# Kernel optimization log

Measured on AMD Instinct MI355X. Metric: run time of the kernel, lower is better.

The kernel has to match this reference:

```python
import jax, jax.numpy as jnp
import numpy as np

B, C_IN, C_OUT, F, K = 4, 64, 64, 50000, 16
BN_EPS = 1e-5


def setup_inputs() -> dict:
    key = jax.random.key(0)
    k1, k2, k3, k4 = jax.random.split(key, 4)
    fea = jax.random.normal(k1, (B, C_IN, F), dtype=jnp.float32)
    ring_n = jax.random.randint(k2, (B, F, K), 0, F, dtype=jnp.int64)
    # Conv1d(kernel_size=1) weight [out, in] and bias [out]
    W = jax.random.normal(k3, (C_OUT, C_IN), dtype=jnp.float32) / np.sqrt(C_IN)
    b = jax.random.normal(k4, (C_OUT,), dtype=jnp.float32) * 0.01
    gamma = jnp.ones((C_OUT,), dtype=jnp.float32)
    beta = jnp.zeros((C_OUT,), dtype=jnp.float32)
    return {"fea": fea, "ring_n": ring_n, "W": W, "b": b, "gamma": gamma, "beta": beta}


def reference(fea, ring_n, W, b, gamma, beta):
    # Note: original torch code overwrites the cat result, so only the
    # NEIGHBOR features are summed (center face excluded).
    def gather_sum(f, r):  # f: [C, F], r: [F, K]
        return f[:, r].sum(axis=-1)  # [C, F, K] -> [C, F]

    summed = jax.vmap(gather_sum)(fea, ring_n)  # [B, C_in, F]
    # 1x1 conv == channel matmul
    y = jnp.einsum("oc,bcf->bof", W, summed) + b[None, :, None]  # [B, C_out, F]
    # BatchNorm1d (training mode): stats over (batch, faces) per channel
    mean = y.mean(axis=(0, 2), keepdims=True)
    var = y.var(axis=(0, 2), keepdims=True)  # biased, as torch BN uses for normalization
    y = (y - mean) * jax.lax.rsqrt(var + BN_EPS)
    y = y * gamma[None, :, None] + beta[None, :, None]
    return jax.nn.relu(y)
```

## Files before the change

kernel.cpp:

```cpp
#include <hip/hip_runtime.h>
#include <hip/hip_bf16.h>
#include <stdint.h>

#define Bn 4
#define Cn 64
#define Fn 50000
#define Kn 16
#define NTOT (Bn*Fn)
#define EPS 1e-5f

typedef unsigned short u16;
typedef unsigned int u32;
typedef __attribute__((ext_vector_type(8))) short short8;
typedef __attribute__((ext_vector_type(4))) float f32x4;

__device__ __forceinline__ u16 f2bf(float x) {
  __hip_bfloat16 h = __float2bfloat16(x);
  return *reinterpret_cast<u16*>(&h);
}
__device__ __forceinline__ u32 pack2(float a, float b) {
  return (u32)f2bf(a) | ((u32)f2bf(b) << 16);
}
__device__ __forceinline__ void gload_lds16(const float* g, float* l) {
  __builtin_amdgcn_global_load_lds(
      (const __attribute__((address_space(1))) u32*)(g),
      (__attribute__((address_space(3))) u32*)(l), 16, 0, 0);
}

__global__ __launch_bounds__(256) void k1_mfma(
    const float* __restrict__ fea, const float* __restrict__ W,
    u32* __restrict__ Gt, float* __restrict__ gsum) {
  const int b = blockIdx.y;
  const int f0 = blockIdx.x * 128;
  const int t = threadIdx.x;
  const int l = t & 63;
  const int quad = l >> 4;
  const int lane15 = l & 15;
  const int wv = t >> 6;
  __shared__ float a_s[64 * 128];

  if (blockIdx.x == 0 && b == 0 && t < 128) gsum[t] = 0.f;

  {
    const float* fb = fea + (size_t)b * Cn * Fn;
    #pragma unroll
    for (int i = 0; i < 8; i++) {
      const int ch = wv * 16 + 2 * i + (l >> 5);
      const int fblk = (l & 31) ^ ((((ch >> 3) & 3)) << 1);
      int fg = f0 + fblk * 4;
      if (fg >= Fn) fg = f0;
      gload_lds16(fb + (size_t)ch * Fn + fg, &a_s[(wv * 16 + 2 * i) * 128]);
    }
  }

  short8 afr[4][2];
  #pragma unroll
  for (int ot = 0; ot < 4; ot++) {
    #pragma unroll
    for (int kk = 0; kk < 2; kk++) {
      const float* wr = W + (ot * 16 + lane15) * 64 + kk * 32 + quad * 8;
      float4 wa = *(const float4*)wr;
      float4 wb = *(const float4*)(wr + 4);
      union { short8 v; u32 u[4]; } fr;
      fr.u[0] = pack2(wa.x, wa.y); fr.u[1] = pack2(wa.z, wa.w);
      fr.u[2] = pack2(wb.x, wb.y); fr.u[3] = pack2(wb.z, wb.w);
      afr[ot][kk] = fr.v;
    }
  }
  __syncthreads();

  f32x4 acc[4][2];
  #pragma unroll
  for (int ot = 0; ot < 4; ot++)
    #pragma unroll
    for (int ft = 0; ft < 2; ft++) acc[ot][ft] = (f32x4){0.f, 0.f, 0.f, 0.f};

  #pragma unroll
  for (int ft = 0; ft < 2; ft++) {
    const int fl = wv * 32 + ft * 16 + lane15;
    const int fsw = fl ^ (quad << 3);
    float x[16];
    #pragma unroll
    for (int j = 0; j < 8; j++) x[j] = a_s[(quad * 8 + j) * 128 + fsw];
    #pragma unroll
    for (int j = 0; j < 8; j++) x[8 + j] = a_s[(32 + quad * 8 + j) * 128 + fsw];
    union { short8 s; u32 u[4]; } b0, b1;
    #pragma unroll
    for (int p = 0; p < 4; p++) {
      b0.u[p] = pack2(x[2 * p], x[2 * p + 1]);
      b1.u[p] = pack2(x[8 + 2 * p], x[8 + 2 * p + 1]);
    }
    #pragma unroll
    for (int ot = 0; ot < 4; ot++) {
      acc[ot][ft] = __builtin_amdgcn_mfma_f32_16x16x32_bf16(afr[ot][0], b0.s, acc[ot][ft], 0, 0, 0);
      acc[ot][ft] = __builtin_amdgcn_mfma_f32_16x16x32_bf16(afr[ot][1], b1.s, acc[ot][ft], 0, 0, 0);
    }
  }

  #pragma unroll
  for (int ot = 0; ot < 4; ot++) {
    #pragma unroll
    for (int ft = 0; ft < 2; ft++) {
      int fg = f0 + wv * 32 + ft * 16 + lane15;
      if (fg < Fn) {
        uint2 pv;
        pv.x = pack2(acc[ot][ft][0], acc[ot][ft][1]);
        pv.y = pack2(acc[ot][ft][2], acc[ot][ft][3]);
        *(uint2*)(Gt + ((size_t)(b * 4 + ot) * Fn + fg) * 8 + quad * 2) = pv;
      }
    }
  }
}

template<int WRITE_BF16>
__global__ __launch_bounds__(256) void k2_gather(
    const u32* __restrict__ Gt, const int* __restrict__ ring,
    const float* __restrict__ bias, u32* __restrict__ Y, float* __restrict__ outF,
    float* __restrict__ gsum, float* __restrict__ gsum2) {
  const int bid = blockIdx.x;
  const int combo = bid & 15;
  const int ft = bid >> 4;
  const int b = combo >> 2;
  const int seg = combo & 3;
  const int t = threadIdx.x;
  const int face_l = t >> 1;
  const int half = t & 1;
  const int fa = ft * 128 + face_l;
  const bool valid = fa < Fn;

  __shared__ float y_s[128][17];
  __shared__ float rs[16][17];
  __shared__ float rs2[16][17];

  float acc[8];
  #pragma unroll
  for (int i = 0; i < 8; i++) acc[i] = 0.f;

  const int c0 = seg * 16 + half * 8;
  float bv[8];
  #pragma unroll
  for (int i = 0; i < 8; i++) bv[i] = bias[c0 + i];

  if (valid) {
    const int4* rp = (const int4*)(ring + ((size_t)b * Fn + fa) * Kn);
    int4 i0 = rp[0], i1 = rp[1], i2 = rp[2], i3 = rp[3];
    int idx[16] = {i0.x,i0.y,i0.z,i0.w, i1.x,i1.y,i1.z,i1.w,
                   i2.x,i2.y,i2.z,i2.w, i3.x,i3.y,i3.z,i3.w};
    const uint4* Gs = (const uint4*)(Gt + (size_t)combo * Fn * 8);
    uint4 v[8], w[8];
    #pragma unroll
    for (int k = 0; k < 8; k++) v[k] = Gs[(size_t)idx[k] * 2 + half];
    #pragma unroll
    for (int k = 0; k < 8; k++) w[k] = Gs[(size_t)idx[8 + k] * 2 + half];
    #pragma unroll
    for (int k = 0; k < 8; k++) {
      u32 uu[4] = {v[k].x, v[k].y, v[k].z, v[k].w};
      #pragma unroll
      for (int p = 0; p < 4; p++) {
        acc[2*p]   += __uint_as_float(uu[p] << 16);
        acc[2*p+1] += __uint_as_float(uu[p] & 0xffff0000u);
      }
    }
    #pragma unroll
    for (int k = 0; k < 8; k++) {
      u32 uu[4] = {w[k].x, w[k].y, w[k].z, w[k].w};
      #pragma unroll
      for (int p = 0; p < 4; p++) {
        acc[2*p]   += __uint_as_float(uu[p] << 16);
        acc[2*p+1] += __uint_as_float(uu[p] & 0xffff0000u);
      }
    }
  }
  #pragma unroll
  for (int i = 0; i < 8; i++) acc[i] = valid ? acc[i] + bv[i] : 0.f;
  #pragma unroll
  for (int i = 0; i < 8; i++) y_s[face_l][half * 8 + i] = acc[i];
  __syncthreads();

  if (WRITE_BF16) {
    const int fp = t & 63, chb = t >> 6;
    const int fa2 = ft * 64 + fp;
    if (fa2 * 2 < Fn) {
      #pragma unroll
      for (int j = 0; j < 4; j++) {
        int ch = chb * 4 + j;
        Y[((size_t)b * 64 + seg * 16 + ch) * (Fn / 2) + fa2] =
            pack2(y_s[fp * 2][ch], y_s[fp * 2 + 1][ch]);
      }
    }
  } else {
    const int fl2 = t & 127, chb = t >> 7;
    if (ft * 128 + fl2 < Fn) {
      float* ob = outF + ((size_t)b * 64 + seg * 16 + chb * 8) * Fn + ft * 128 + fl2;
      #pragma unroll
      for (int j = 0; j < 8; j++) ob[(size_t)j * Fn] = y_s[fl2][chb * 8 + j];
    }
  }

  {
    const int ch = t & 15, part = t >> 4;
    float s = 0.f, s2 = 0.f;
    #pragma unroll
    for (int i = 0; i < 8; i++) {
      float v = y_s[part * 8 + i][ch];
      s += v; s2 += v * v;
    }
    rs[part][ch] = s; rs2[part][ch] = s2;
  }
  __syncthreads();
  if (t < 16) {
    float s = 0.f;
    #pragma unroll
    for (int p = 0; p < 16; p++) s += rs[p][t];
    atomicAdd(&gsum[seg * 16 + t], s);
  } else if (t < 32) {
    const int ch = t - 16;
    float s2 = 0.f;
    #pragma unroll
    for (int p = 0; p < 16; p++) s2 += rs2[p][ch];
    atomicAdd(&gsum2[seg * 16 + ch], s2);
  }
}

__global__ void k3_stats(const float* __restrict__ gsum, const float* __restrict__ gsum2,
                         const float* __restrict__ gamma, const float* __restrict__ beta,
                         float* __restrict__ ab) {
  int o = threadIdx.x;
  if (o < 64) {
    float inv = 1.0f / (float)NTOT;
    float mean = gsum[o] * inv;
    float var = gsum2[o] * inv - mean * mean;
    float r = rsqrtf(var + EPS);
    float a = gamma[o] * r;
    ab[o] = a;
    ab[64 + o] = beta[o] - mean * a;
  }
}

__global__ __launch_bounds__(256) void k4_norm_bf(
    const u32* __restrict__ Y, const float* __restrict__ gsum,
    const float* __restrict__ gsum2, const float* __restrict__ gamma,
    const float* __restrict__ beta, float* __restrict__ out) {
  int i = blockIdx.x * 256 + threadIdx.x;
  int ch = (i / 12500) & 63;
  const float inv = 1.0f / (float)NTOT;
  float mean = gsum[ch] * inv;
  float var = gsum2[ch] * inv - mean * mean;
  float a = gamma[ch] * rsqrtf(var + EPS);
  float cc = beta[ch] - mean * a;
  uint2 u = ((const uint2*)Y)[i];
  float4 v;
  v.x = fmaxf(fmaf(__uint_as_float(u.x << 16), a, cc), 0.f);
  v.y = fmaxf(fmaf(__uint_as_float(u.x & 0xffff0000u), a, cc), 0.f);
  v.z = fmaxf(fmaf(__uint_as_float(u.y << 16), a, cc), 0.f);
  v.w = fmaxf(fmaf(__uint_as_float(u.y & 0xffff0000u), a, cc), 0.f);
  ((float4*)out)[i] = v;
}

__global__ __launch_bounds__(256) void k4_norm_f32(float* __restrict__ out,
                                                   const float* __restrict__ ab) {
  int i = blockIdx.x * 256 + threadIdx.x;
  int o = (i / (Fn / 4)) & 63;
  float a = ab[o], c = ab[64 + o];
  float4 v = ((float4*)out)[i];
  v.x = fmaxf(fmaf(v.x, a, c), 0.f);
  v.y = fmaxf(fmaf(v.y, a, c), 0.f);
  v.z = fmaxf(fmaf(v.z, a, c), 0.f);
  v.w = fmaxf(fmaf(v.w, a, c), 0.f);
  ((float4*)out)[i] = v;
}

extern "C" void kernel_launch(void* const* d_in, const int* in_sizes, int n_in,
                              void* d_out, int out_size, void* d_ws, size_t ws_size,
                              hipStream_t stream) {
  const float* fea   = (const float*)d_in[0];
  const int*   ring  = (const int*)d_in[1];
  const float* W     = (const float*)d_in[2];
  const float* bias  = (const float*)d_in[3];
  const float* gamma = (const float*)d_in[4];
  const float* beta  = (const float*)d_in[5];
  float* out = (float*)d_out;

  u32* Gt = (u32*)d_ws;
  const size_t gtBytes = (size_t)Bn * 4 * Fn * 8 * 4;
  const size_t yBytes  = (size_t)Bn * 64 * (Fn / 2) * 4;
  const bool bf16y = ws_size >= gtBytes + yBytes + 1024;

  u32* Y = (u32*)((char*)d_ws + gtBytes);
  float* gsum  = bf16y ? (float*)((char*)d_ws + gtBytes + yBytes)
                       : (float*)((char*)d_ws + gtBytes);
  float* gsum2 = gsum + 64;
  float* ab    = gsum + 128;

  k1_mfma<<<dim3((Fn + 127) / 128, Bn), 256, 0, stream>>>(fea, W, Gt, gsum);
  const int ftiles = (Fn + 127) / 128;
  if (bf16y) {
    k2_gather<1><<<dim3(ftiles * 16), 256, 0, stream>>>(Gt, ring, bias, Y, out, gsum, gsum2);
    k4_norm_bf<<<dim3(Bn * 64 * 12500 / 256), 256, 0, stream>>>(Y, gsum, gsum2, gamma, beta, out);
  } else {
    k2_gather<0><<<dim3(ftiles * 16), 256, 0, stream>>>(Gt, ring, bias, Y, out, gsum, gsum2);
    k3_stats<<<1, 64, 0, stream>>>(gsum, gsum2, gamma, beta, ab);
    k4_norm_f32<<<dim3((Bn * Cn * Fn / 4) / 256), 256, 0, stream>>>(out, ab);
  }
}
```

Measured before the change: 190.4 us.

## Make gather kernel persistent over face tiles with ring-index prefetch

The gather kernel now launches a fixed grid of 2048 blocks, each looping over a contiguous range of 128-face tiles instead of handling a single tile. Ring indices for the next tile are prefetched while the current one is processed. Per-thread running sums and sums of squares are kept across tiles, and the block reduction plus global atomics run once per block rather than once per tile. This cuts block-launch overhead and atomic traffic, but adds two barriers per tile and leaves fewer independent waves to hide gather latency.

Measured after the change: 194.5 us. +2.2%, slower.

```diff
diff --git a/kernel.cpp b/kernel.cpp
--- a/kernel.cpp
+++ b/kernel.cpp
@@ -119,93 +119,135 @@
     float* __restrict__ gsum, float* __restrict__ gsum2) {
   const int bid = blockIdx.x;
   const int combo = bid & 15;
-  const int ft = bid >> 4;
+  const int sub = bid >> 4;
   const int b = combo >> 2;
   const int seg = combo & 3;
   const int t = threadIdx.x;
   const int face_l = t >> 1;
   const int half = t & 1;
-  const int fa = ft * 128 + face_l;
-  const bool valid = fa < Fn;
 
   __shared__ float y_s[128][17];
   __shared__ float rs[16][17];
   __shared__ float rs2[16][17];
 
-  float acc[8];
-  #pragma unroll
-  for (int i = 0; i < 8; i++) acc[i] = 0.f;
-
   const int c0 = seg * 16 + half * 8;
   float bv[8];
   #pragma unroll
   for (int i = 0; i < 8; i++) bv[i] = bias[c0 + i];
 
-  if (valid) {
-    const int4* rp = (const int4*)(ring + ((size_t)b * Fn + fa) * Kn);
-    int4 i0 = rp[0], i1 = rp[1], i2 = rp[2], i3 = rp[3];
-    int idx[16] = {i0.x,i0.y,i0.z,i0.w, i1.x,i1.y,i1.z,i1.w,
-                   i2.x,i2.y,i2.z,i2.w, i3.x,i3.y,i3.z,i3.w};
-    const uint4* Gs = (const uint4*)(Gt + (size_t)combo * Fn * 8);
-    uint4 v[8], w[8];
-    #pragma unroll
-    for (int k = 0; k < 8; k++) v[k] = Gs[(size_t)idx[k] * 2 + half];
-    #pragma unroll
-    for (int k = 0; k < 8; k++) w[k] = Gs[(size_t)idx[8 + k] * 2 + half];
-    #pragma unroll
-    for (int k = 0; k < 8; k++) {
-      u32 uu[4] = {v[k].x, v[k].y, v[k].z, v[k].w};
+  const int NT = (Fn + 127) / 128;
+  const int t_begin = sub * NT / 128;
+  const int t_end = (sub + 1) * NT / 128;
+
+  float sacc[8], s2acc[8];
+  #pragma unroll
+  for (int i = 0; i < 8; i++) { sacc[i] = 0.f; s2acc[i] = 0.f; }
+
+  const uint4* Gs = (const uint4*)(Gt + (size_t)combo * Fn * 8);
+  const int* rbase = ring + (size_t)b * Fn * Kn;
+
+  int4 r0, r1, r2, r3;
+  {
+    int fa = t_begin * 128 + face_l;
+    int fc = fa < Fn ? fa : 0;
+    const int4* rp = (const int4*)(rbase + (size_t)fc * Kn);
+    r0 = rp[0]; r1 = rp[1]; r2 = rp[2]; r3 = rp[3];
+  }
+
+  for (int tile = t_begin; tile < t_end; ++tile) {
+    const int fa = tile * 128 + face_l;
+    const bool valid = fa < Fn;
+    int idx[16] = {r0.x,r0.y,r0.z,r0.w, r1.x,r1.y,r1.z,r1.w,
+                   r2.x,r2.y,r2.z,r2.w, r3.x,r3.y,r3.z,r3.w};
+
+    if (tile + 1 < t_end) {
+      int nfa = (tile + 1) * 128 + face_l;
+      int nfc = nfa < Fn ? nfa : 0;
+      const int4* rp = (const int4*)(rbase + (size_t)nfc * Kn);
+      r0 = rp[0]; r1 = rp[1]; r2 = rp[2]; r3 = rp[3];
+    }
+
+    float acc[8];
+    #pragma unroll
+    for (int i = 0; i < 8; i++) acc[i] = 0.f;
+
+    if (valid) {
+      uint4 v[8], w[8];
       #pragma unroll
-      for (int p = 0; p < 4; p++) {
-        acc[2*p]   += __uint_as_float(uu[p] << 16);
-        acc[2*p+1] += __uint_as_float(uu[p] & 0xffff0000u);
-      }
-    }
-    #pragma unroll
-    for (int k = 0; k < 8; k++) {
-      u32 uu[4] = {w[k].x, w[k].y, w[k].z, w[k].w};
+      for (int k = 0; k < 8; k++) v[k] = Gs[(size_t)idx[k] * 2 + half];
       #pragma unroll
-      for (int p = 0; p < 4; p++) {
-        acc[2*p]   += __uint_as_float(uu[p] << 16);
-        acc[2*p+1] += __uint_as_float(uu[p] & 0xffff0000u);
-      }
-    }
-  }
-  #pragma unroll
-  for (int i = 0; i < 8; i++) acc[i] = valid ? acc[i] + bv[i] : 0.f;
-  #pragma unroll
-  for (int i = 0; i < 8; i++) y_s[face_l][half * 8 + i] = acc[i];
-  __syncthreads();
-
-  if (WRITE_BF16) {
-    const int fp = t & 63, chb = t >> 6;
-    const int fa2 = ft * 64 + fp;
-    if (fa2 * 2 < Fn) {
+      for (int k = 0; k < 8; k++) w[k] = Gs[(size_t)idx[8 + k] * 2 + half];
       #pragma unroll
-      for (int j = 0; j < 4; j++) {
-        int ch = chb * 4 + j;
-        Y[((size_t)b * 64 + seg * 16 + ch) * (Fn / 2) + fa2] =
-            pack2(y_s[fp * 2][ch], y_s[fp * 2 + 1][ch]);
-      }
-    }
-  } else {
-    const int fl2 = t & 127, chb = t >> 7;
-    if (ft * 128 + fl2 < Fn) {
-      float* ob = outF + ((size_t)b * 64 + seg * 16 + chb * 8) * Fn + ft * 128 + fl2;
+      for (int k = 0; k < 8; k++) {
+        u32 uu[4] = {v[k].x, v[k].y, v[k].z, v[k].w};
+        #pragma unroll
+        for (int p = 0; p < 4; p++) {
+          acc[2*p]   += __uint_as_float(uu[p] << 16);
+          acc[2*p+1] += __uint_as_float(uu[p] & 0xffff0000u);
+        }
+      }
       #pragma unroll
-      for (int j = 0; j < 8; j++) ob[(size_t)j * Fn] = y_s[fl2][chb * 8 + j];
-    }
-  }
-
+      for (int k = 0; k < 8; k++) {
+        u32 uu[4] = {w[k].x, w[k].y, w[k].z, w[k].w};
+        #pragma unroll
+        for (int p = 0; p < 4; p++) {
+          acc[2*p]   += __uint_as_float(uu[p] << 16);
+          acc[2*p+1] += __uint_as_float(uu[p] & 0xffff0000u);
+        }
+      }
+    }
+    #pragma unroll
+    for (int i = 0; i < 8; i++) acc[i] = valid ? acc[i] + bv[i] : 0.f;
+    #pragma unroll
+    for (int i = 0; i < 8; i++) {
+      sacc[i] += acc[i];
+      s2acc[i] += acc[i] * acc[i];
+    }
+    #pragma unroll
+    for (int i = 0; i < 8; i++) y_s[face_l][half * 8 + i] = acc[i];
+    __syncthreads();
+
+    if (WRITE_BF16) {
+      const int fp = t & 63, chb = t >> 6;
+      const int fa2 = tile * 64 + fp;
+      if (fa2 * 2 < Fn) {
+        #pragma unroll
+        for (int j = 0; j < 4; j++) {
+          int ch = chb * 4 + j;
+          Y[((size_t)b * 64 + seg * 16 + ch) * (Fn / 2) + fa2] =
+              pack2(y_s[fp * 2][ch], y_s[fp * 2 + 1][ch]);
+        }
+      }
+    } else {
+      const int fl2 = t & 127, chb = t >> 7;
+      if (tile * 128 + fl2 < Fn) {
+        float* ob = outF + ((size_t)b * 64 + seg * 16 + chb * 8) * Fn + tile * 128 + fl2;
+        #pragma unroll
+        for (int j = 0; j < 8; j++) ob[(size_t)j * Fn] = y_s[fl2][chb * 8 + j];
+      }
+    }
+    __syncthreads();
+  }
+
+  const int ch = t & 15, part = t >> 4;
+  #pragma unroll
+  for (int i = 0; i < 8; i++) y_s[face_l][half * 8 + i] = sacc[i];
+  __syncthreads();
   {
-    const int ch = t & 15, part = t >> 4;
-    float s = 0.f, s2 = 0.f;
-    #pragma unroll
-    for (int i = 0; i < 8; i++) {
-      float v = y_s[part * 8 + i][ch];
-      s += v; s2 += v * v;
-    }
-    rs[part][ch] = s; rs2[part][ch] = s2;
+    float s = 0.f;
+    #pragma unroll
+    for (int i = 0; i < 8; i++) s += y_s[part * 8 + i][ch];
+    rs[part][ch] = s;
+  }
+  __syncthreads();
+  #pragma unroll
+  for (int i = 0; i < 8; i++) y_s[face_l][half * 8 + i] = s2acc[i];
+  __syncthreads();
+  {
+    float s2 = 0.f;
+    #pragma unroll
+    for (int i = 0; i < 8; i++) s2 += y_s[part * 8 + i][ch];
+    rs2[part][ch] = s2;
   }
   __syncthreads();
   if (t < 16) {
@@ -214,11 +256,11 @@
     for (int p = 0; p < 16; p++) s += rs[p][t];
     atomicAdd(&gsum[seg * 16 + t], s);
   } else if (t < 32) {
-    const int ch = t - 16;
+    const int ch2 = t - 16;
     float s2 = 0.f;
     #pragma unroll
-    for (int p = 0; p < 16; p++) s2 += rs2[p][ch];
-    atomicAdd(&gsum2[seg * 16 + ch], s2);
+    for (int p = 0; p < 16; p++) s2 += rs2[p][ch2];
+    atomicAdd(&gsum2[seg * 16 + ch2], s2);
   }
 }
 
@@ -293,12 +335,11 @@
   float* ab    = gsum + 128;
 
   k1_mfma<<<dim3((Fn + 127) / 128, Bn), 256, 0, stream>>>(fea, W, Gt, gsum);
-  const int ftiles = (Fn + 127) / 128;
   if (bf16y) {
-    k2_gather<1><<<dim3(ftiles * 16), 256, 0, stream>>>(Gt, ring, bias, Y, out, gsum, gsum2);
+    k2_gather<1><<<dim3(2048), 256, 0, stream>>>(Gt, ring, bias, Y, out, gsum, gsum2);
     k4_norm_bf<<<dim3(Bn * 64 * 12500 / 256), 256, 0, stream>>>(Y, gsum, gsum2, gamma, beta, out);
   } else {
-    k2_gather<0><<<dim3(ftiles * 16), 256, 0, stream>>>(Gt, ring, bias, Y, out, gsum, gsum2);
+    k2_gather<0><<<dim3(2048), 256, 0, stream>>>(Gt, ring, bias, Y, out, gsum, gsum2);
     k3_stats<<<1, 64, 0, stream>>>(gsum, gsum2, gamma, beta, ab);
     k4_norm_f32<<<dim3((Bn * Cn * Fn / 4) / 256), 256, 0, stream>>>(out, ab);
   }
```
